# Kernel tuning notes

Hardware: AMD Instinct MI355X
Metric: run time of the kernel (lower is better)

Reference implementation:

```python
import jax, jax.numpy as jnp
import numpy as np

B, C, H, W = 16, 64, 48, 48
D = C * W  # xLSTM embedding dim (== C*H since H==W)
K = 5          # phi='S' kernel size
G_CONV = C // 8  # conv groups = 8
G_NORM = 16      # GroupNorm groups
EPS = 1e-5


def setup_inputs() -> dict:
    key = jax.random.key(0)
    ks = jax.random.split(key, 10)
    s = 0.02
    return {
        'x': jax.random.normal(ks[0], (B, C, H, W), jnp.float32),
        'W1': (jax.random.normal(ks[1], (D, 4 * D), jnp.float32) * s),
        'R1': (jax.random.normal(ks[2], (D, 4 * D), jnp.float32) * s),
        'b1': jnp.zeros((4 * D,), jnp.float32),
        'W2': (jax.random.normal(ks[3], (D, 4 * D), jnp.float32) * s),
        'R2': (jax.random.normal(ks[4], (D, 4 * D), jnp.float32) * s),
        'b2': jnp.zeros((4 * D,), jnp.float32),
        'conv_w': jax.random.normal(ks[5], (C, C // G_CONV, K), jnp.float32) * (1.0 / np.sqrt((C // G_CONV) * K)),
        'gn_gamma': jnp.ones((C,), jnp.float32),
        'gn_beta': jnp.zeros((C,), jnp.float32),
    }


def xlstm_stack(x, Wm, Rm, bm):
    """sLSTM-style xLSTM block (exp gating + stabilizer). x: [B,T,D] -> [B,T,D]."""
    Bsz, T, Dm = x.shape
    pre = jnp.einsum('btd,de->bte', x, Wm) + bm  # input projection for all steps

    def step(carry, p):
        h, c, n, m = carry
        g = p + h @ Rm                      # [B,4D]
        it, ft, zt, ot = jnp.split(g, 4, axis=-1)
        m_new = jnp.maximum(ft + m, it)     # stabilizer
        i = jnp.exp(it - m_new)
        f = jnp.exp(ft + m - m_new)
        c_new = f * c + i * jnp.tanh(zt)
        n_new = f * n + i
        h_new = jax.nn.sigmoid(ot) * c_new / (n_new + 1e-6)
        return (h_new, c_new, n_new, m_new), h_new

    z = jnp.zeros((Bsz, Dm), x.dtype)
    _, ys = jax.lax.scan(step, (z, z, z, z), jnp.swapaxes(pre, 0, 1))
    return jnp.swapaxes(ys, 0, 1)  # [B,T,D]


def conv1d_grouped(x, w):
    pad = K // 2
    return jax.lax.conv_general_dilated(
        x, w, window_strides=(1,), padding=[(pad, pad)],
        feature_group_count=G_CONV, dimension_numbers=('NCH', 'OIH', 'NCH'))


def group_norm(x, gamma, beta):
    b, c, L = x.shape
    xg = x.reshape(b, G_NORM, -1)
    mu = xg.mean(-1, keepdims=True)
    var = xg.var(-1, keepdims=True)
    xn = ((xg - mu) * jax.lax.rsqrt(var + EPS)).reshape(b, c, L)
    return xn * gamma[None, :, None] + beta[None, :, None]


def ela_forward(x, W1, R1, b1, W2, R2, b2, conv_w, gn_gamma, gn_beta):
    b, c, h, w = x.shape
    # stack cfg2: sequence over h, features c*w
    y2 = xlstm_stack(x.reshape(b, h, c * w), W2, R2, b2).reshape(b, c, w, h)
    # stack cfg1: sequence over w, features c*h
    y1 = xlstm_stack(x.reshape(b, w, c * h), W1, R1, b1).reshape(b, c, w, h)
    x_h = jnp.mean(y2, axis=3).reshape(b, c, h)
    x_w = jnp.mean(y1, axis=2).reshape(b, c, w)
    x_h = jax.nn.sigmoid(group_norm(conv1d_grouped(x_h, conv_w), gn_gamma, gn_beta)).reshape(b, c, h, 1)
    x_w = jax.nn.sigmoid(group_norm(conv1d_grouped(x_w, conv_w), gn_gamma, gn_beta)).reshape(b, c, 1, w)
    return x_h * x_w * x


def reference(x, W1, R1, b1, W2, R2, b2, conv_w, gn_gamma, gn_beta):
    return ela_forward(x, W1, R1, b1, W2, R2, b2, conv_w, gn_gamma, gn_beta)
```

## Files before the change

### kernel.cpp

```cpp
#include <hip/hip_runtime.h>
#include <hip/hip_bf16.h>


typedef float  f32x4 __attribute__((ext_vector_type(4)));
typedef __bf16 v8bf  __attribute__((ext_vector_type(8)));
typedef __bf16 v4bf  __attribute__((ext_vector_type(4)));

#define MFMA16(a, b, c) __builtin_amdgcn_mfma_f32_16x16x32_bf16((a), (b), (c), 0, 0, 0)

static constexpr size_t OFF_PREP = 0;
static constexpr size_t SZ_PREP  = 37748736;
static constexpr size_t OFF_H0   = 37748736;
static constexpr size_t OFF_H1   = 37945344;
static constexpr size_t OFF_C    = 38141952;
static constexpr size_t OFF_N    = 38535168;
static constexpr size_t OFF_M    = 38928384;
static constexpr size_t OFF_YS   = 39321600;
static constexpr size_t OFF_GATE = 39714816;
static constexpr size_t BASE_END = 40108032;
static constexpr size_t SZ_RPACK = 75497472;
static constexpr size_t OFF_RA   = BASE_END;
static constexpr size_t OFF_RB   = BASE_END + SZ_RPACK;
static constexpr size_t END_A    = OFF_RB + SZ_RPACK;

__device__ __forceinline__ void gl_lds16(const void* g, void* l) {
    __builtin_amdgcn_global_load_lds(
        (const __attribute__((address_space(1))) unsigned int*)g,
        (__attribute__((address_space(3))) unsigned int*)l, 16, 0, 0);
}

__global__ __launch_bounds__(256) void zero_kernel(f32x4* __restrict__ p, int n) {
    int i = blockIdx.x * 256 + threadIdx.x;
    if (i < n) { f32x4 z = 0.0f; p[i] = z; }
}

__global__ __launch_bounds__(256) void pack_x_kernel(const float* __restrict__ x,
                                                     __bf16* __restrict__ dst) {
    int gi = blockIdx.x * 256 + threadIdx.x;
    int lane = gi & 63;
    int rest = gi >> 6;
    int sub = rest & 7; rest >>= 3;
    int kc = rest % 96, mb = rest / 96;
    int r = mb * 128 + sub * 16 + (lane & 15);
    int t = r >> 4, b = r & 15;
    int k = kc * 32 + (lane >> 4) * 8;
    const f32x4* s = (const f32x4*)(x + (size_t)b * 147456 + (size_t)t * 3072 + k);
    f32x4 v0 = s[0], v1 = s[1];
    v8bf o;
#pragma unroll
    for (int j = 0; j < 4; ++j) { o[j] = (__bf16)v0[j]; o[4 + j] = (__bf16)v1[j]; }
    ((v8bf*)dst)[gi] = o;
}

__global__ __launch_bounds__(256) void pack_B_kernel(const float* __restrict__ src0,
                                                     const float* __restrict__ src1,
                                                     __bf16* __restrict__ dst0,
                                                     __bf16* __restrict__ dst1) {
    int nb = blockIdx.x, kc = blockIdx.y, m = blockIdx.z;
    const float* src = m ? src1 : src0;
    __bf16* dst = m ? dst1 : dst0;
    int tid = threadIdx.x;
    __shared__ float tile[32][133];
    int kr = tid >> 3, nc0 = (tid & 7) * 16;
    const f32x4* s4 = (const f32x4*)(src + (size_t)(kc * 32 + kr) * 12288 + nb * 128 + nc0);
    f32x4 v0 = s4[0], v1 = s4[1], v2 = s4[2], v3 = s4[3];
#pragma unroll
    for (int r = 0; r < 4; ++r) {
        tile[kr][nc0 + r]      = v0[r];
        tile[kr][nc0 + 4 + r]  = v1[r];
        tile[kr][nc0 + 8 + r]  = v2[r];
        tile[kr][nc0 + 12 + r] = v3[r];
    }
    __syncthreads();
    __bf16* db = dst + (size_t)(nb * 96 + kc) * 4096;
#pragma unroll
    for (int c = 0; c < 2; ++c) {
        int lidx = tid * 2 + c;
        int sub = lidx >> 6, lane = lidx & 63;
        int kb = (lane >> 4) * 8, nn = sub * 16 + (lane & 15);
        v8bf o;
#pragma unroll
        for (int j = 0; j < 8; ++j) o[j] = (__bf16)tile[kb + j][nn];
        ((v8bf*)db)[lidx] = o;
    }
}

__global__ __launch_bounds__(256) void pre_gemm(const __bf16* __restrict__ Apack,
                                                const float* __restrict__ W1,
                                                const float* __restrict__ W2,
                                                __bf16* __restrict__ preP) {
    int nb = blockIdx.x, mb = blockIdx.y, stack = blockIdx.z;
    const float* W = stack ? W2 : W1;
    int tid = threadIdx.x, wave = tid >> 6, lane = tid & 63;
    __shared__ alignas(16) __bf16 As[4096];
    __shared__ alignas(16) __bf16 Bs[4096];
    __shared__ float tile[32][133];
    f32x4 acc[4][4];
#pragma unroll
    for (int i = 0; i < 4; ++i)
#pragma unroll
        for (int j = 0; j < 4; ++j) acc[i][j] = 0.0f;

    int kr = tid >> 3, nc0 = (tid & 7) * 16;
    for (int kc = 0; kc < 96; ++kc) {
        size_t atile = (size_t)(mb * 96 + kc) * 8192;
        int chunk = wave * 2048;
        gl_lds16((const char*)Apack + atile + chunk + lane * 16,        (char*)As + chunk);
        gl_lds16((const char*)Apack + atile + chunk + 1024 + lane * 16, (char*)As + chunk + 1024);
        const f32x4* s4 = (const f32x4*)(W + (size_t)(kc * 32 + kr) * 12288 + nb * 128 + nc0);
        f32x4 v0 = s4[0], v1 = s4[1], v2 = s4[2], v3 = s4[3];
#pragma unroll
        for (int r = 0; r < 4; ++r) {
            tile[kr][nc0 + r]      = v0[r];
            tile[kr][nc0 + 4 + r]  = v1[r];
            tile[kr][nc0 + 8 + r]  = v2[r];
            tile[kr][nc0 + 12 + r] = v3[r];
        }
        __syncthreads();
#pragma unroll
        for (int c = 0; c < 2; ++c) {
            int lidx = tid * 2 + c;
            int sub = lidx >> 6, l2 = lidx & 63;
            int kb = (l2 >> 4) * 8, nn = sub * 16 + (l2 & 15);
            v8bf o;
#pragma unroll
            for (int j = 0; j < 8; ++j) o[j] = (__bf16)tile[kb + j][nn];
            ((v8bf*)Bs)[lidx] = o;
        }
        __syncthreads();
        const v8bf* A8 = (const v8bf*)As;
        const v8bf* B8 = (const v8bf*)Bs;
        v8bf a[4], b[4];
#pragma unroll
        for (int mi = 0; mi < 4; ++mi) a[mi] = A8[((wave >> 1) * 4 + mi) * 64 + lane];
#pragma unroll
        for (int ni = 0; ni < 4; ++ni) b[ni] = B8[((wave & 1) * 4 + ni) * 64 + lane];
#pragma unroll
        for (int mi = 0; mi < 4; ++mi)
#pragma unroll
            for (int ni = 0; ni < 4; ++ni) acc[mi][ni] = MFMA16(a[mi], b[ni], acc[mi][ni]);
        __syncthreads();
    }
#pragma unroll
    for (int mi = 0; mi < 4; ++mi)
#pragma unroll
        for (int ni = 0; ni < 4; ++ni) {
            int mt = mb * 8 + (wave >> 1) * 4 + mi;
            int nt4 = nb * 8 + (wave & 1) * 4 + ni;
            v4bf o;
#pragma unroll
            for (int r = 0; r < 4; ++r) o[r] = (__bf16)acc[mi][ni][r];
            ((v4bf*)preP)[(((size_t)stack * 48 + mt) * 768 + nt4) * 64 + lane] = o;
        }
}

__global__ __launch_bounds__(256) void step_kernel(
    const __bf16* __restrict__ Rp0, const __bf16* __restrict__ Rp1,
    const __bf16* __restrict__ hread, __bf16* __restrict__ hwrite,
    const __bf16* __restrict__ preP,
    const float* __restrict__ bias1, const float* __restrict__ bias2,
    float* __restrict__ cbuf, float* __restrict__ nbuf, float* __restrict__ mbuf,
    float* __restrict__ ysum, int t) {
    int nt = blockIdx.x, stack = blockIdx.y;
    int tid = threadIdx.x, wave = tid >> 6, lane = tid & 63;
    const v8bf* Rp = (const v8bf*)(stack ? Rp1 : Rp0);
    const v8bf* hA = (const v8bf*)hread + (size_t)stack * 96 * 64;
    int sub = nt & 7;
    size_t base[4];
#pragma unroll
    for (int i = 0; i < 4; ++i) {
        int nb = i * 24 + (nt >> 3);
        base[i] = (size_t)nb * 49152 + (size_t)sub * 64 + lane;
    }
    int kcs = wave * 24;
    f32x4 acc[4];
#pragma unroll
    for (int i = 0; i < 4; ++i) acc[i] = 0.0f;

    v8bf a0 = hA[(size_t)kcs * 64 + lane];
    v8bf bf[4];
#pragma unroll
    for (int i = 0; i < 4; ++i) bf[i] = Rp[base[i] + (size_t)kcs * 512];
    for (int kk = 0; kk < 24; ++kk) {
        v8bf a1 = a0;
        v8bf bn[4];
        if (kk < 23) {
            int kc1 = kcs + kk + 1;
            a1 = hA[(size_t)kc1 * 64 + lane];
#pragma unroll
            for (int i = 0; i < 4; ++i) bn[i] = Rp[base[i] + (size_t)kc1 * 512];
        } else {
#pragma unroll
            for (int i = 0; i < 4; ++i) bn[i] = bf[i];
        }
#pragma unroll
        for (int i = 0; i < 4; ++i) acc[i] = MFMA16(a0, bf[i], acc[i]);
        a0 = a1;
#pragma unroll
        for (int i = 0; i < 4; ++i) bf[i] = bn[i];
    }

    __shared__ f32x4 red4[4][4][64];
#pragma unroll
    for (int i = 0; i < 4; ++i) red4[wave][i][lane] = acc[i];
    __syncthreads();

    if (wave == 0) {
        const float* bias = stack ? bias2 : bias1;
        f32x4 g[4];
#pragma unroll
        for (int i = 0; i < 4; ++i)
            g[i] = red4[0][i][lane] + red4[1][i][lane] + red4[2][i][lane] + red4[3][i][lane];
        int fcol = nt * 16 + (lane & 15);
        int bq = (lane >> 4) * 4;
#pragma unroll
        for (int i = 0; i < 4; ++i) {
            v4bf pv = ((const v4bf*)preP)[(((size_t)stack * 48 + t) * 768 + (i * 192 + nt)) * 64 + lane];
            float bv = bias[i * 3072 + fcol];
#pragma unroll
            for (int r = 0; r < 4; ++r) g[i][r] += (float)pv[r] + bv;
        }
        size_t sidx = ((size_t)stack * 192 + nt) * 64 + lane;
        f32x4 cc = ((f32x4*)cbuf)[sidx];
        f32x4 nn = ((f32x4*)nbuf)[sidx];
        f32x4 mm = ((f32x4*)mbuf)[sidx];
        int kc = fcol >> 5, ko = fcol & 31;
        __bf16* hw = hwrite + ((size_t)stack * 96 + kc) * 512 + (size_t)(ko >> 3) * 128 + (ko & 7);
        int flat = t * 3072 + fcol;
        int cch = flat / 2304;
        int rem = flat - cch * 2304;
        int u = rem / 48;
        int v = rem - u * 48;
        int yidx = cch * 48 + (stack ? u : v);
        float* yb = ysum + (size_t)stack * 16 * 3072;
#pragma unroll
        for (int r = 0; r < 4; ++r) {
            int brow = bq + r;
            float it = g[0][r], ft = g[1][r], zt = g[2][r], ot = g[3][r];
            float mnew = fmaxf(ft + mm[r], it);
            float iv = __expf(it - mnew);
            float fv = __expf(ft + mm[r] - mnew);
            float cnew = fv * cc[r] + iv * tanhf(zt);
            float nnew = fv * nn[r] + iv;
            float sg = 1.0f / (1.0f + __expf(-ot));
            float h = sg * cnew / (nnew + 1e-6f);
            cc[r] = cnew; nn[r] = nnew; mm[r] = mnew;
            hw[(size_t)brow * 8] = (__bf16)h;
            atomicAdd(yb + (size_t)brow * 3072 + yidx, h);
        }
        ((f32x4*)cbuf)[sidx] = cc;
        ((f32x4*)nbuf)[sidx] = nn;
        ((f32x4*)mbuf)[sidx] = mm;
    }
}

__global__ __launch_bounds__(256) void conv_gn_kernel(const float* __restrict__ ysum,
                                                      const float* __restrict__ cw,
                                                      const float* __restrict__ gamma,
                                                      const float* __restrict__ beta,
                                                      float* __restrict__ gatebuf) {
    int bi = blockIdx.x;
    int s = bi >> 4, b = bi & 15;
    int tid = threadIdx.x;
    __shared__ float in0[3072], cvout[3072], cws[2560];
    __shared__ float r1[16][16], r2[16][16], mu_s[16], rs_s[16];
    const float* src = ysum + (size_t)(s * 16 + b) * 3072;
    for (int e = tid; e < 3072; e += 256) in0[e] = src[e] * (1.0f / 48.0f);
    for (int e = tid; e < 2560; e += 256) cws[e] = cw[e];
    __syncthreads();
    for (int e = tid; e < 3072; e += 256) {
        int co = e / 48, p = e - co * 48;
        int g = co >> 3;
        const float* wrow = cws + co * 40;
        const float* irow = in0 + g * 8 * 48;
        float a = 0.f;
#pragma unroll
        for (int ci = 0; ci < 8; ++ci)
#pragma unroll
            for (int q = 0; q < 5; ++q) {
                int pp = p + q - 2;
                if (pp >= 0 && pp < 48) a += wrow[ci * 5 + q] * irow[ci * 48 + pp];
            }
        cvout[e] = a;
    }
    __syncthreads();
    int gn = tid >> 4, ln = tid & 15;
    float s1 = 0.f, s2 = 0.f;
    for (int ii = ln; ii < 192; ii += 16) {
        float v = cvout[gn * 192 + ii];
        s1 += v; s2 += v * v;
    }
    r1[gn][ln] = s1; r2[gn][ln] = s2;
    __syncthreads();
    if (tid < 16) {
        float a = 0.f, c2 = 0.f;
        for (int ii = 0; ii < 16; ++ii) { a += r1[tid][ii]; c2 += r2[tid][ii]; }
        float mu = a * (1.0f / 192.0f);
        float var = c2 * (1.0f / 192.0f) - mu * mu;
        mu_s[tid] = mu;
        rs_s[tid] = rsqrtf(var + 1e-5f);
    }
    __syncthreads();
    float* dst = gatebuf + (size_t)(s * 16 + b) * 3072;
    for (int e = tid; e < 3072; e += 256) {
        int c = e / 48;
        int gg = c >> 2;
        float xn = (cvout[e] - mu_s[gg]) * rs_s[gg] * gamma[c] + beta[c];
        dst[e] = 1.0f / (1.0f + __expf(-xn));
    }
}

__global__ __launch_bounds__(256) void final_kernel(const float* __restrict__ x,
                                                    const float* __restrict__ gatebuf,
                                                    float* __restrict__ out) {
    int gid = blockIdx.x * 256 + threadIdx.x;
    int wi4 = gid % 12;
    int rest = gid / 12;
    int hi = rest % 48;
    int bc = rest / 48;
    int b = bc >> 6, c = bc & 63;
    f32x4 xv = ((const f32x4*)x)[gid];
    float gh = gatebuf[(size_t)(16 + b) * 3072 + c * 48 + hi];
    f32x4 gw = *(const f32x4*)(gatebuf + (size_t)b * 3072 + c * 48 + wi4 * 4);
    f32x4 o;
#pragma unroll
    for (int k = 0; k < 4; ++k) o[k] = xv[k] * gh * gw[k];
    ((f32x4*)out)[gid] = o;
}

extern "C" void kernel_launch(void* const* d_in, const int* in_sizes, int n_in,
                              void* d_out, int out_size, void* d_ws, size_t ws_size,
                              hipStream_t stream) {
    const float* x     = (const float*)d_in[0];
    const float* W1    = (const float*)d_in[1];
    const float* R1    = (const float*)d_in[2];
    const float* b1    = (const float*)d_in[3];
    const float* W2    = (const float*)d_in[4];
    const float* R2    = (const float*)d_in[5];
    const float* b2    = (const float*)d_in[6];
    const float* cw    = (const float*)d_in[7];
    const float* gamma = (const float*)d_in[8];
    const float* beta  = (const float*)d_in[9];

    char* ws = (char*)d_ws;
    __bf16* seqA = (__bf16*)d_out;
    __bf16* preP = (__bf16*)(ws + OFF_PREP);
    __bf16* h0   = (__bf16*)(ws + OFF_H0);
    __bf16* h1   = (__bf16*)(ws + OFF_H1);
    float* cbuf  = (float*)(ws + OFF_C);
    float* nbuf  = (float*)(ws + OFF_N);
    float* mbuf  = (float*)(ws + OFF_M);
    float* ysum  = (float*)(ws + OFF_YS);
    float* gate  = (float*)(ws + OFF_GATE);

    bool r_in_ws = ws_size >= END_A;
    __bf16* RA = r_in_ws ? (__bf16*)(ws + OFF_RA) : (__bf16*)d_in[1];
    __bf16* RB = r_in_ws ? (__bf16*)(ws + OFF_RB) : (__bf16*)d_in[4];

    pack_x_kernel<<<1152, 256, 0, stream>>>(x, seqA);
    pre_gemm<<<dim3(96, 6, 2), 256, 0, stream>>>(seqA, W1, W2, preP);
    pack_B_kernel<<<dim3(96, 96, 2), 256, 0, stream>>>(R1, R2, RA, RB);
    zero_kernel<<<480, 256, 0, stream>>>((f32x4*)(ws + OFF_H0), 122880);
    for (int t = 0; t < 48; ++t) {
        const __bf16* hr = (t & 1) ? h1 : h0;
        __bf16* hw       = (t & 1) ? h0 : h1;
        step_kernel<<<dim3(192, 2), 256, 0, stream>>>(RA, RB, hr, hw, preP, b1, b2,
                                                      cbuf, nbuf, mbuf, ysum, t);
    }
    conv_gn_kernel<<<32, 256, 0, stream>>>(ysum, cw, gamma, beta, gate);
    final_kernel<<<2304, 256, 0, stream>>>(x, gate, (float*)d_out);
}
```

Measured before the change: 2.653 ms.

## Pre-pack W for input GEMM and split recurrent K across eight waves

```diff
diff --git a/kernel.cpp b/kernel.cpp
--- a/kernel.cpp
+++ b/kernel.cpp
@@ -85,6 +85,56 @@
     }
 }
 
+__global__ __launch_bounds__(256) void pre_gemm_packed(const __bf16* __restrict__ Apack,
+                                                       const __bf16* __restrict__ Bp0,
+                                                       const __bf16* __restrict__ Bp1,
+                                                       __bf16* __restrict__ preP) {
+    int nb = blockIdx.x, mb = blockIdx.y, stack = blockIdx.z;
+    const char* Bpack = (const char*)(stack ? Bp1 : Bp0);
+    int tid = threadIdx.x, wave = tid >> 6, lane = tid & 63;
+    __shared__ alignas(16) __bf16 As[4096];
+    __shared__ alignas(16) __bf16 Bs[4096];
+    f32x4 acc[4][4];
+#pragma unroll
+    for (int i = 0; i < 4; ++i)
+#pragma unroll
+        for (int j = 0; j < 4; ++j) acc[i][j] = 0.0f;
+
+    for (int kc = 0; kc < 96; ++kc) {
+        size_t atile = (size_t)(mb * 96 + kc) * 8192;
+        size_t btile = (size_t)(nb * 96 + kc) * 8192;
+        int chunk = wave * 2048;
+        gl_lds16((const char*)Apack + atile + chunk + lane * 16,        (char*)As + chunk);
+        gl_lds16((const char*)Apack + atile + chunk + 1024 + lane * 16, (char*)As + chunk + 1024);
+        gl_lds16(Bpack + btile + chunk + lane * 16,        (char*)Bs + chunk);
+        gl_lds16(Bpack + btile + chunk + 1024 + lane * 16, (char*)Bs + chunk + 1024);
+        __syncthreads();
+        const v8bf* A8 = (const v8bf*)As;
+        const v8bf* B8 = (const v8bf*)Bs;
+        v8bf a[4], b[4];
+#pragma unroll
+        for (int mi = 0; mi < 4; ++mi) a[mi] = A8[((wave >> 1) * 4 + mi) * 64 + lane];
+#pragma unroll
+        for (int ni = 0; ni < 4; ++ni) b[ni] = B8[((wave & 1) * 4 + ni) * 64 + lane];
+#pragma unroll
+        for (int mi = 0; mi < 4; ++mi)
+#pragma unroll
+            for (int ni = 0; ni < 4; ++ni) acc[mi][ni] = MFMA16(a[mi], b[ni], acc[mi][ni]);
+        __syncthreads();
+    }
+#pragma unroll
+    for (int mi = 0; mi < 4; ++mi)
+#pragma unroll
+        for (int ni = 0; ni < 4; ++ni) {
+            int mt = mb * 8 + (wave >> 1) * 4 + mi;
+            int nt4 = nb * 8 + (wave & 1) * 4 + ni;
+            v4bf o;
+#pragma unroll
+            for (int r = 0; r < 4; ++r) o[r] = (__bf16)acc[mi][ni][r];
+            ((v4bf*)preP)[(((size_t)stack * 48 + mt) * 768 + nt4) * 64 + lane] = o;
+        }
+}
+
 __global__ __launch_bounds__(256) void pre_gemm(const __bf16* __restrict__ Apack,
                                                 const float* __restrict__ W1,
                                                 const float* __restrict__ W2,
@@ -154,7 +204,7 @@
         }
 }
 
-__global__ __launch_bounds__(256) void step_kernel(
+__global__ __launch_bounds__(512) void step_kernel(
     const __bf16* __restrict__ Rp0, const __bf16* __restrict__ Rp1,
     const __bf16* __restrict__ hread, __bf16* __restrict__ hwrite,
     const __bf16* __restrict__ preP,
@@ -172,7 +222,7 @@
         int nb = i * 24 + (nt >> 3);
         base[i] = (size_t)nb * 49152 + (size_t)sub * 64 + lane;
     }
-    int kcs = wave * 24;
+    int kcs = wave * 12;
     f32x4 acc[4];
 #pragma unroll
     for (int i = 0; i < 4; ++i) acc[i] = 0.0f;
@@ -181,10 +231,10 @@
     v8bf bf[4];
 #pragma unroll
     for (int i = 0; i < 4; ++i) bf[i] = Rp[base[i] + (size_t)kcs * 512];
-    for (int kk = 0; kk < 24; ++kk) {
+    for (int kk = 0; kk < 12; ++kk) {
         v8bf a1 = a0;
         v8bf bn[4];
-        if (kk < 23) {
+        if (kk < 11) {
             int kc1 = kcs + kk + 1;
             a1 = hA[(size_t)kc1 * 64 + lane];
 #pragma unroll
@@ -200,7 +250,7 @@
         for (int i = 0; i < 4; ++i) bf[i] = bn[i];
     }
 
-    __shared__ f32x4 red4[4][4][64];
+    __shared__ f32x4 red4[8][4][64];
 #pragma unroll
     for (int i = 0; i < 4; ++i) red4[wave][i][lane] = acc[i];
     __syncthreads();
@@ -209,8 +259,12 @@
         const float* bias = stack ? bias2 : bias1;
         f32x4 g[4];
 #pragma unroll
-        for (int i = 0; i < 4; ++i)
-            g[i] = red4[0][i][lane] + red4[1][i][lane] + red4[2][i][lane] + red4[3][i][lane];
+        for (int i = 0; i < 4; ++i) {
+            f32x4 s = red4[0][i][lane];
+#pragma unroll
+            for (int w = 1; w < 8; ++w) s += red4[w][i][lane];
+            g[i] = s;
+        }
         int fcol = nt * 16 + (lane & 15);
         int bq = (lane >> 4) * 4;
 #pragma unroll
@@ -353,18 +407,24 @@
     float* ysum  = (float*)(ws + OFF_YS);
     float* gate  = (float*)(ws + OFF_GATE);
 
-    bool r_in_ws = ws_size >= END_A;
-    __bf16* RA = r_in_ws ? (__bf16*)(ws + OFF_RA) : (__bf16*)d_in[1];
-    __bf16* RB = r_in_ws ? (__bf16*)(ws + OFF_RB) : (__bf16*)d_in[4];
+    bool big_ws = ws_size >= END_A;
+    __bf16* PA = (__bf16*)(ws + OFF_RA);
+    __bf16* PB = (__bf16*)(ws + OFF_RB);
 
     pack_x_kernel<<<1152, 256, 0, stream>>>(x, seqA);
-    pre_gemm<<<dim3(96, 6, 2), 256, 0, stream>>>(seqA, W1, W2, preP);
-    pack_B_kernel<<<dim3(96, 96, 2), 256, 0, stream>>>(R1, R2, RA, RB);
+    if (big_ws) {
+        pack_B_kernel<<<dim3(96, 96, 2), 256, 0, stream>>>(W1, W2, PA, PB);
+        pre_gemm_packed<<<dim3(96, 6, 2), 256, 0, stream>>>(seqA, PA, PB, preP);
+        pack_B_kernel<<<dim3(96, 96, 2), 256, 0, stream>>>(R1, R2, PA, PB);
+    } else {
+        pre_gemm<<<dim3(96, 6, 2), 256, 0, stream>>>(seqA, W1, W2, preP);
+        pack_B_kernel<<<dim3(96, 96, 2), 256, 0, stream>>>(R1, R2, PA, PB);
+    }
     zero_kernel<<<480, 256, 0, stream>>>((f32x4*)(ws + OFF_H0), 122880);
     for (int t = 0; t < 48; ++t) {
         const __bf16* hr = (t & 1) ? h1 : h0;
         __bf16* hw       = (t & 1) ? h0 : h1;
-        step_kernel<<<dim3(192, 2), 256, 0, stream>>>(RA, RB, hr, hw, preP, b1, b2,
+        step_kernel<<<dim3(192, 2), 512, 0, stream>>>(PA, PB, hr, hw, preP, b1, b2,
                                                       cbuf, nbuf, mbuf, ysum, t);
     }
     conv_gn_kernel<<<32, 256, 0, stream>>>(ysum, cw, gamma, beta, gate);
```

After: 2.692 ms. No clear change (+1.4%).
